# Kernel optimization log

Measured on AMD Instinct MI355X. Metric: run time of the kernel, lower is better.

Reference implementation:

```python
import jax, jax.numpy as jnp
import numpy as np

N, E, G = 50000, 800000, 64          # nodes, edges, graphs in batch
H, C = 4, 32                          # heads, per-head channels
D = H * C                             # 128 = gat_hidden_dim * n_heads
EMB = 16
IN_DIM = 2 * EMB + 1                  # 33
LSTM_H = 256
OUT = 4
V_LAB, V_TYP = 1000, 100
EPS = 1e-5


def _gatv2(x, src, dst, Wl, bl, Wr, br, att, bias):
    # GATv2Conv (PyG semantics, self-loops already appended to src/dst).
    xl = (x @ Wl + bl).reshape(-1, H, C)   # lin_l -> source-side messages x_j
    xr = (x @ Wr + br).reshape(-1, H, C)   # lin_r -> target-side x_i
    xj = xl[src]                            # [Et, H, C]
    e = jax.nn.leaky_relu(xr[dst] + xj, 0.2)
    score = jnp.einsum('ehc,hc->eh', e, att)             # [Et, H]
    smax = jax.ops.segment_max(score, dst, num_segments=N)
    a = jnp.exp(score - smax[dst])
    denom = jax.ops.segment_sum(a, dst, num_segments=N)
    alpha = a / denom[dst]                                # scatter-softmax per dst
    out = jax.ops.segment_sum(xj * alpha[:, :, None], dst, num_segments=N)
    return out.reshape(N, D) + bias


def _graph_norm(x, batch_ids, w, b, ms):
    # PyG GraphNorm: per-graph mean (scaled by learnable ms) and variance.
    cnt = jax.ops.segment_sum(jnp.ones((N,), x.dtype), batch_ids, num_segments=G)[:, None]
    mean = jax.ops.segment_sum(x, batch_ids, num_segments=G) / cnt
    out = x - mean[batch_ids] * ms
    var = jax.ops.segment_sum(out * out, batch_ids, num_segments=G) / cnt
    return w * out / jnp.sqrt(var + EPS)[batch_ids] + b


def _lstm0(x, Wih, Whh, bih, bhh):
    # Single LSTM time-step with h0 = c0 = 0: the Whh @ h0 term vanishes,
    # the forget gate multiplies c0 = 0.  Gate order (PyTorch): i, f, g, o.
    g = x @ Wih.T + bih + bhh
    i, f, gg, o = jnp.split(g, 4, axis=-1)
    c = jax.nn.sigmoid(i) * jnp.tanh(gg)
    return jax.nn.sigmoid(o) * jnp.tanh(c)


def setup_inputs() -> dict:
    key = jax.random.key(0)
    ks = jax.random.split(key, 32)
    rn = lambda k, s, sc=0.05: jax.random.normal(k, s, jnp.float32) * sc
    Z4 = LSTM_H * 4
    return {
        'node_labels': jax.random.randint(ks[0], (N,), 0, V_LAB, jnp.int32),
        'node_types': jax.random.randint(ks[1], (N,), 0, V_TYP, jnp.int32),
        'node_feat': jax.random.normal(ks[2], (N, 1), jnp.float32),
        'edge_index': jax.random.randint(ks[3], (2, E), 0, N, jnp.int32),
        'batch_ids': jnp.sort(jax.random.randint(ks[4], (N,), 0, G, jnp.int32)),
        'emb_label': rn(ks[5], (V_LAB, EMB), 1.0),
        'emb_type': rn(ks[6], (V_TYP, EMB), 1.0),
        'W_in': rn(ks[7], (IN_DIM, D)), 'b_in': jnp.zeros((D,), jnp.float32),
        'g1_Wl': rn(ks[8], (D, D)), 'g1_bl': jnp.zeros((D,), jnp.float32),
        'g1_Wr': rn(ks[9], (D, D)), 'g1_br': jnp.zeros((D,), jnp.float32),
        'g1_att': rn(ks[10], (H, C), 0.1), 'g1_bias': jnp.zeros((D,), jnp.float32),
        'gn1_w': jnp.ones((D,), jnp.float32), 'gn1_b': jnp.zeros((D,), jnp.float32),
        'gn1_ms': jnp.ones((D,), jnp.float32),
        'g2_Wl': rn(ks[11], (D, D)), 'g2_bl': jnp.zeros((D,), jnp.float32),
        'g2_Wr': rn(ks[12], (D, D)), 'g2_br': jnp.zeros((D,), jnp.float32),
        'g2_att': rn(ks[13], (H, C), 0.1), 'g2_bias': jnp.zeros((D,), jnp.float32),
        'gn2_w': jnp.ones((D,), jnp.float32), 'gn2_b': jnp.zeros((D,), jnp.float32),
        'gn2_ms': jnp.ones((D,), jnp.float32),
        'W_res': rn(ks[14], (D, D)), 'b_res': jnp.zeros((D,), jnp.float32),
        'l1_Wih': rn(ks[15], (Z4, D)), 'l1_Whh': rn(ks[16], (Z4, LSTM_H)),
        'l1_bih': jnp.zeros((Z4,), jnp.float32), 'l1_bhh': jnp.zeros((Z4,), jnp.float32),
        'l2_Wih': rn(ks[17], (Z4, LSTM_H)), 'l2_Whh': rn(ks[18], (Z4, LSTM_H)),
        'l2_bih': jnp.zeros((Z4,), jnp.float32), 'l2_bhh': jnp.zeros((Z4,), jnp.float32),
        'ln_w': jnp.ones((LSTM_H,), jnp.float32), 'ln_b': jnp.zeros((LSTM_H,), jnp.float32),
        'fc_W': rn(ks[19], (LSTM_H, OUT)), 'fc_b': jnp.zeros((OUT,), jnp.float32),
    }


def reference(node_labels, node_types, node_feat, edge_index, batch_ids,
              emb_label, emb_type, W_in, b_in,
              g1_Wl, g1_bl, g1_Wr, g1_br, g1_att, g1_bias, gn1_w, gn1_b, gn1_ms,
              g2_Wl, g2_bl, g2_Wr, g2_br, g2_att, g2_bias, gn2_w, gn2_b, gn2_ms,
              W_res, b_res,
              l1_Wih, l1_Whh, l1_bih, l1_bhh, l2_Wih, l2_Whh, l2_bih, l2_bhh,
              ln_w, ln_b, fc_W, fc_b):
    # Node features: [label_emb | type_emb | scalar]  -> [N, 33]
    feat = jnp.concatenate([emb_label[node_labels], emb_type[node_types], node_feat], axis=1)
    # PositionalEncoding at position 0 with odd d_model=33 adds exactly zeros (no-op).
    x = feat @ W_in + b_in                                  # [N, D]

    loops = jnp.arange(N, dtype=edge_index.dtype)           # GATv2Conv add_self_loops=True
    src = jnp.concatenate([edge_index[0], loops])
    dst = jnp.concatenate([edge_index[1], loops])

    x1 = jax.nn.elu(_graph_norm(_gatv2(x, src, dst, g1_Wl, g1_bl, g1_Wr, g1_br, g1_att, g1_bias),
                                batch_ids, gn1_w, gn1_b, gn1_ms))
    # dropout = identity in eval mode
    x2 = jax.nn.elu(_graph_norm(_gatv2(x1, src, dst, g2_Wl, g2_bl, g2_Wr, g2_br, g2_att, g2_bias),
                                batch_ids, gn2_w, gn2_b, gn2_ms) + x1 @ W_res + b_res)

    h1 = _lstm0(x2, l1_Wih, l1_Whh, l1_bih, l1_bhh)         # seq_len = 1 LSTM
    h2 = _lstm0(h1, l2_Wih, l2_Whh, l2_bih, l2_bhh)

    mu = h2.mean(-1, keepdims=True)
    var = ((h2 - mu) ** 2).mean(-1, keepdims=True)
    hn = ln_w * (h2 - mu) / jnp.sqrt(var + EPS) + ln_b      # LayerNorm

    cnt = jax.ops.segment_sum(jnp.ones((N,), hn.dtype), batch_ids, num_segments=G)[:, None]
    pooled = jax.ops.segment_sum(hn, batch_ids, num_segments=G) / cnt  # global_mean_pool
    return jax.nn.log_softmax(pooled @ fc_W + fc_b, axis=1)            # [G, OUT]
```

## Files before the change

### kernel.cpp

```cpp
#include <hip/hip_runtime.h>
#include <cstdint>
#include <cstddef>

#define DD 128
#define LSTMH 256
#define ZG 1024

typedef __attribute__((ext_vector_type(8))) short short8v;
typedef __attribute__((ext_vector_type(4))) float float4v;

static inline int cdiv_(int a, int b) { return (a + b - 1) / b; }

__device__ __forceinline__ float sigm_(float x) { return 1.f / (1.f + __expf(-x)); }
__device__ __forceinline__ float tanh_(float x) {
  float e = __expf(-2.f * fabsf(x));
  float r = (1.f - e) / (1.f + e);
  return copysignf(r, x);
}

__device__ __forceinline__ unsigned short f2bf(float f) {
  uint32_t u = __float_as_uint(f);
  u += 0x7fffu + ((u >> 16) & 1u);
  return (unsigned short)(u >> 16);
}
__device__ __forceinline__ uint32_t bfpack(float a, float b) {
  return (uint32_t)f2bf(a) | ((uint32_t)f2bf(b) << 16);
}
__device__ __forceinline__ float bflo(uint32_t u) { return __uint_as_float(u << 16); }
__device__ __forceinline__ float bfhi(uint32_t u) { return __uint_as_float(u & 0xffff0000u); }

__global__ void prep_all(const float* __restrict__ g1Wl, const float* __restrict__ g1Wr,
                         const float* __restrict__ g2Wl, const float* __restrict__ g2Wr,
                         const float* __restrict__ Wres, const float* __restrict__ l1Wih,
                         const float* __restrict__ l2Wih, const float* __restrict__ g1bl,
                         const float* __restrict__ g1br, const float* __restrict__ g2bl,
                         const float* __restrict__ g2br, const float* __restrict__ bres,
                         const float* __restrict__ l1bih, const float* __restrict__ l1bhh,
                         const float* __restrict__ l2bih, const float* __restrict__ l2bhh,
                         unsigned short* __restrict__ wcat1, unsigned short* __restrict__ wcat2,
                         unsigned short* __restrict__ wl1b, unsigned short* __restrict__ wl2b,
                         float* __restrict__ bcat1, float* __restrict__ bcat2,
                         float* __restrict__ bsum1, float* __restrict__ bsum2) {
  int i = blockIdx.x * 256 + threadIdx.x;
  if (i < 81920) {
    int seg = i >> 14, j = i & 16383;
    int m = j >> 7, k = j & 127;
    const float* src = (seg == 0) ? g1Wl : (seg == 1) ? g1Wr : (seg == 2) ? g2Wl
                       : (seg == 3) ? g2Wr : Wres;
    unsigned short* dst = (seg == 0) ? wcat1 : (seg == 1) ? wcat1 + 16384
                          : (seg == 2) ? wcat2 : (seg == 3) ? wcat2 + 16384 : wcat2 + 32768;
    dst[j] = f2bf(src[k * 128 + m]);
    return;
  }
  i -= 81920;
  if (i < 131072) { wl1b[i] = f2bf(l1Wih[i]); return; }
  i -= 131072;
  if (i < 262144) { wl2b[i] = f2bf(l2Wih[i]); return; }
  i -= 262144;
  if (i < 256) { bcat1[i] = (i < 128) ? g1bl[i] : g1br[i - 128]; return; }
  i -= 256;
  if (i < 384) {
    bcat2[i] = (i < 128) ? g2bl[i] : (i < 256 ? g2br[i - 128] : bres[i - 256]);
    return;
  }
  i -= 384;
  if (i < 1024) { bsum1[i] = l1bih[i] + l1bhh[i]; return; }
  i -= 1024;
  if (i < 1024) { bsum2[i] = l2bih[i] + l2bhh[i]; return; }
}

__global__ __launch_bounds__(256) void embed_in2(
    const int* __restrict__ labels, const int* __restrict__ types,
    const float* __restrict__ nf, const float* __restrict__ embL,
    const float* __restrict__ embT, const float* __restrict__ W,
    const float* __restrict__ b, unsigned short* __restrict__ x, int N) {
  __shared__ float f[128][34];
  int base = blockIdx.x * 128;
  int tid = threadIdx.x;
  int ch = tid & 127, half = tid >> 7;
  float wr[33];
#pragma unroll
  for (int k = 0; k < 33; ++k) wr[k] = W[k * 128 + ch];
  float bb = b[ch];
  int nmax = N - base < 128 ? N - base : 128;
  for (int e = tid; e < nmax * 32; e += 256) {
    int n = e >> 5, k = e & 31;
    f[n][k] = (k < 16) ? embL[labels[base + n] * 16 + k] : embT[types[base + n] * 16 + (k - 16)];
  }
  for (int n = tid; n < nmax; n += 256) f[n][32] = nf[base + n];
  __syncthreads();
  for (int n = half; n < nmax; n += 2) {
    float acc = bb;
#pragma unroll
    for (int k = 0; k < 33; ++k) acc = fmaf(f[n][k], wr[k], acc);
    x[(size_t)(base + n) * 128 + ch] = f2bf(acc);
  }
}

__global__ void count_deg(const int* __restrict__ ei, int* __restrict__ deg, int E_, int N_) {
  int i = blockIdx.x * 256 + threadIdx.x;
  if (i < E_) atomicAdd(&deg[ei[E_ + i]], 1);
  else if (i < E_ + N_) atomicAdd(&deg[i - E_], 1);
}

__global__ __launch_bounds__(256) void scan1(const int* __restrict__ deg, int* __restrict__ offs,
                                             int* __restrict__ partials, int N_) {
  __shared__ int buf[2][256];
  int tid = threadIdx.x;
  int i = blockIdx.x * 256 + tid;
  int v = (i < N_) ? deg[i] : 0;
  buf[0][tid] = v;
  __syncthreads();
  int cur = 0;
#pragma unroll
  for (int d = 1; d < 256; d <<= 1) {
    int xv = buf[cur][tid];
    if (tid >= d) xv += buf[cur][tid - d];
    buf[cur ^ 1][tid] = xv;
    cur ^= 1;
    __syncthreads();
  }
  int incl = buf[cur][tid];
  if (i < N_) offs[i] = incl - v;
  if (tid == 255) partials[blockIdx.x] = incl;
}

__global__ __launch_bounds__(256) void scan2(int* __restrict__ partials, int* __restrict__ offs,
                                             int nb, int N_) {
  __shared__ int buf[2][256];
  int tid = threadIdx.x;
  int v = (tid < nb) ? partials[tid] : 0;
  buf[0][tid] = v;
  __syncthreads();
  int cur = 0;
#pragma unroll
  for (int d = 1; d < 256; d <<= 1) {
    int xv = buf[cur][tid];
    if (tid >= d) xv += buf[cur][tid - d];
    buf[cur ^ 1][tid] = xv;
    cur ^= 1;
    __syncthreads();
  }
  int incl = buf[cur][tid];
  if (tid < nb) partials[tid] = incl - v;
  if (tid == 255) offs[N_] = incl;
}

__global__ void scan3(int* __restrict__ offs, const int* __restrict__ partials, int N_) {
  int i = blockIdx.x * 256 + threadIdx.x;
  if (i < N_) offs[i] += partials[blockIdx.x];
}

__global__ void fill_csr(const int* __restrict__ ei, const int* __restrict__ offs,
                         int* __restrict__ cursor, int* __restrict__ csr, int E_, int N_) {
  int i = blockIdx.x * 256 + threadIdx.x;
  int s, d;
  if (i < E_) { s = ei[i]; d = ei[E_ + i]; }
  else if (i < E_ + N_) { s = d = i - E_; }
  else return;
  int pos = offs[d] + atomicAdd(&cursor[d], 1);
  csr[pos] = s;
}

__global__ void graph_ranges(const int* __restrict__ bids, int* __restrict__ gstart,
                             float* __restrict__ invcnt, int N_, int G_) {
  int t = threadIdx.x;
  if (t <= G_) {
    int lo = 0, hi = N_;
    while (lo < hi) { int mid = (lo + hi) >> 1; if (bids[mid] < t) lo = mid + 1; else hi = mid; }
    gstart[t] = lo;
  }
  __syncthreads();
  if (t < G_) {
    int c = gstart[t + 1] - gstart[t];
    invcnt[t] = (c > 0) ? 1.f / (float)c : 0.f;
  }
}

__global__ __launch_bounds__(256) void gemm_bf16(
    const unsigned short* __restrict__ A, const unsigned short* __restrict__ Bp,
    const float* __restrict__ bias, unsigned short* __restrict__ C, int M, int K, int Ncols) {
  __shared__ unsigned short As[128 * 40];
  __shared__ unsigned short Bs[128 * 40];
  int tid = threadIdx.x;
  int lane = tid & 63;
  int wid = tid >> 6;
  int rowBase = blockIdx.y * 128, colBase = blockIdx.x * 128;
  int wr = (wid >> 1) * 64, wc = (wid & 1) * 64;
  int fr = lane & 15, fg = lane >> 4;
  float4v acc[4][4];
#pragma unroll
  for (int i = 0; i < 4; ++i)
#pragma unroll
    for (int j = 0; j < 4; ++j) acc[i][j] = (float4v){0.f, 0.f, 0.f, 0.f};

  int sr = tid >> 2;
  int sc = tid & 3;
  int off_lo = (sc < 2) ? 32 * sc : 32 * sc - 56;

  for (int k0 = 0; k0 < K; k0 += 32) {
#pragma unroll
    for (int it = 0; it < 2; ++it) {
      int r = it * 64 + sr;
      uint4 va = make_uint4(0u, 0u, 0u, 0u);
      if (rowBase + r < M)
        va = *(const uint4*)(A + (size_t)(rowBase + r) * K + k0 + sc * 8);
      char* arow = (char*)(As + r * 40);
      *(uint2*)(arow + off_lo) = make_uint2(va.x, va.y);
      *(uint2*)(arow + off_lo + 16) = make_uint2(va.z, va.w);
      uint4 vb = *(const uint4*)(Bp + (size_t)(colBase + r) * K + k0 + sc * 8);
      char* brow = (char*)(Bs + r * 40);
      *(uint2*)(brow + off_lo) = make_uint2(vb.x, vb.y);
      *(uint2*)(brow + off_lo + 16) = make_uint2(vb.z, vb.w);
    }
    __syncthreads();
    short8v af[4], bfv[4];
#pragma unroll
    for (int i = 0; i < 4; ++i)
      af[i] = *(const short8v*)((const char*)As + (wr + 16 * i + fr) * 80 + fg * 16);
#pragma unroll
    for (int j = 0; j < 4; ++j)
      bfv[j] = *(const short8v*)((const char*)Bs + (wc + 16 * j + fr) * 80 + fg * 16);
#pragma unroll
    for (int i = 0; i < 4; ++i)
#pragma unroll
      for (int j = 0; j < 4; ++j)
        acc[i][j] = __builtin_amdgcn_mfma_f32_16x16x32_bf16(af[i], bfv[j], acc[i][j], 0, 0, 0);
    __syncthreads();
  }
#pragma unroll
  for (int j = 0; j < 4; ++j) {
    int gc = colBase + wc + 16 * j + fr;
    float bv = bias[gc];
#pragma unroll
    for (int i = 0; i < 4; ++i) {
      int gr0 = rowBase + wr + 16 * i + fg * 4;
#pragma unroll
      for (int rg = 0; rg < 4; ++rg) {
        int gr = gr0 + rg;
        if (gr < M) C[(size_t)gr * Ncols + gc] = f2bf(acc[i][j][rg] + bv);
      }
    }
  }
}

__global__ __launch_bounds__(256) void gat_agg(
    const unsigned short* __restrict__ xlr, int stride,
    const int* __restrict__ csr, const int* __restrict__ offs,
    const float* __restrict__ att, const float* __restrict__ bias,
    unsigned short* __restrict__ out, int N) {
  int wid = (blockIdx.x * 256 + threadIdx.x) >> 6;
  if (wid >= N) return;
  int lane = threadIdx.x & 63;
  int q = lane >> 4, ql = lane & 15;
  float4 aA = *(const float4*)&att[ql * 8];
  float4 aB = *(const float4*)&att[ql * 8 + 4];
  uint4 ur = *(const uint4*)(xlr + (size_t)wid * stride + 128 + ql * 8);
  float r0 = bflo(ur.x), r1 = bfhi(ur.x), r2 = bflo(ur.y), r3 = bfhi(ur.y);
  float r4 = bflo(ur.z), r5 = bfhi(ur.z), r6 = bflo(ur.w), r7 = bfhi(ur.w);
  float m = -1e30f, L = 0.f;
  float s0 = 0.f, s1 = 0.f, s2 = 0.f, s3 = 0.f, s4 = 0.f, s5 = 0.f, s6 = 0.f, s7 = 0.f;
  int js = offs[wid], je = offs[wid + 1];
  for (int j = js + q; j < je; j += 4) {
    int s = csr[j];
    uint4 u = *(const uint4*)(xlr + (size_t)s * stride + ql * 8);
    float x0 = bflo(u.x), x1 = bfhi(u.x), x2 = bflo(u.y), x3 = bfhi(u.y);
    float x4 = bflo(u.z), x5 = bfhi(u.z), x6 = bflo(u.w), x7 = bfhi(u.w);
    float v0 = fmaxf(r0 + x0, 0.2f * (r0 + x0));
    float v1 = fmaxf(r1 + x1, 0.2f * (r1 + x1));
    float v2 = fmaxf(r2 + x2, 0.2f * (r2 + x2));
    float v3 = fmaxf(r3 + x3, 0.2f * (r3 + x3));
    float v4 = fmaxf(r4 + x4, 0.2f * (r4 + x4));
    float v5 = fmaxf(r5 + x5, 0.2f * (r5 + x5));
    float v6 = fmaxf(r6 + x6, 0.2f * (r6 + x6));
    float v7 = fmaxf(r7 + x7, 0.2f * (r7 + x7));
    float p = aA.x * v0 + aA.y * v1 + aA.z * v2 + aA.w * v3 +
              aB.x * v4 + aB.y * v5 + aB.z * v6 + aB.w * v7;
    p += __shfl_xor(p, 1); p += __shfl_xor(p, 2);
    float mn = fmaxf(m, p);
    float ea = __expf(p - mn);
    float es = __expf(m - mn);
    L = L * es + ea;
    s0 = s0 * es + ea * x0; s1 = s1 * es + ea * x1;
    s2 = s2 * es + ea * x2; s3 = s3 * es + ea * x3;
    s4 = s4 * es + ea * x4; s5 = s5 * es + ea * x5;
    s6 = s6 * es + ea * x6; s7 = s7 * es + ea * x7;
    m = mn;
  }
#pragma unroll
  for (int d = 16; d <= 32; d <<= 1) {
    float mo = __shfl_xor(m, d), Lo = __shfl_xor(L, d);
    float t0 = __shfl_xor(s0, d), t1 = __shfl_xor(s1, d);
    float t2 = __shfl_xor(s2, d), t3 = __shfl_xor(s3, d);
    float t4 = __shfl_xor(s4, d), t5 = __shfl_xor(s5, d);
    float t6 = __shfl_xor(s6, d), t7 = __shfl_xor(s7, d);
    float mn = fmaxf(m, mo);
    float e0 = __expf(m - mn), e1 = __expf(mo - mn);
    L = L * e0 + Lo * e1;
    s0 = s0 * e0 + t0 * e1; s1 = s1 * e0 + t1 * e1;
    s2 = s2 * e0 + t2 * e1; s3 = s3 * e0 + t3 * e1;
    s4 = s4 * e0 + t4 * e1; s5 = s5 * e0 + t5 * e1;
    s6 = s6 * e0 + t6 * e1; s7 = s7 * e0 + t7 * e1;
    m = mn;
  }
  if (q == 0) {
    float inv = 1.f / L;
    float4 bA = *(const float4*)&bias[ql * 8];
    float4 bB = *(const float4*)&bias[ql * 8 + 4];
    uint4 ov;
    ov.x = bfpack(s0 * inv + bA.x, s1 * inv + bA.y);
    ov.y = bfpack(s2 * inv + bA.z, s3 * inv + bA.w);
    ov.z = bfpack(s4 * inv + bB.x, s5 * inv + bB.y);
    ov.w = bfpack(s6 * inv + bB.z, s7 * inv + bB.w);
    *(uint4*)(out + (size_t)wid * DD + ql * 8) = ov;
  }
}

__global__ __launch_bounds__(256) void gn_stats2(const unsigned short* __restrict__ x,
                                                 const int* __restrict__ bids,
                                                 float* __restrict__ gsum,
                                                 float* __restrict__ gsq, int N) {
  int base = blockIdx.x * 128;
  int cp = threadIdx.x & 63;
  int sub = threadIdx.x >> 6;
  int end = base + 128 < N ? base + 128 : N;
  int curg = -1;
  float s0 = 0.f, s1 = 0.f, q0 = 0.f, q1 = 0.f;
  for (int r = base + sub; r < end; r += 4) {
    int g = bids[r];
    if (g != curg) {
      if (curg >= 0) {
        atomicAdd(&gsum[curg * DD + cp * 2], s0);
        atomicAdd(&gsum[curg * DD + cp * 2 + 1], s1);
        atomicAdd(&gsq[curg * DD + cp * 2], q0);
        atomicAdd(&gsq[curg * DD + cp * 2 + 1], q1);
      }
      curg = g; s0 = s1 = q0 = q1 = 0.f;
    }
    uint32_t u = *(const uint32_t*)(x + (size_t)r * DD + cp * 2);
    float v0 = bflo(u), v1 = bfhi(u);
    s0 += v0; q0 += v0 * v0; s1 += v1; q1 += v1 * v1;
  }
  if (curg >= 0) {
    atomicAdd(&gsum[curg * DD + cp * 2], s0);
    atomicAdd(&gsum[curg * DD + cp * 2 + 1], s1);
    atomicAdd(&gsq[curg * DD + cp * 2], q0);
    atomicAdd(&gsq[curg * DD + cp * 2 + 1], q1);
  }
}

template <bool ADDRES>
__global__ void gn_apply(const unsigned short* __restrict__ xin,
                         unsigned short* __restrict__ xout,
                         const unsigned short* __restrict__ res, int resStride,
                         const int* __restrict__ bids, const float* __restrict__ gsum,
                         const float* __restrict__ gsq, const float* __restrict__ invcnt,
                         const float* __restrict__ w, const float* __restrict__ b,
                         const float* __restrict__ ms, int N) {
  int idx = blockIdx.x * 256 + threadIdx.x;
  if (idx >= N * 64) return;
  int n = idx >> 6, cp = idx & 63;
  int g = bids[n];
  float ic = invcnt[g];
  float2 sm = *(const float2*)&gsum[g * DD + cp * 2];
  float2 sq = *(const float2*)&gsq[g * DD + cp * 2];
  float2 w2 = *(const float2*)&w[cp * 2];
  float2 b2 = *(const float2*)&b[cp * 2];
  float2 m2 = *(const float2*)&ms[cp * 2];
  uint32_t u = *(const uint32_t*)(xin + (size_t)n * DD + cp * 2);
  float mean0 = sm.x * ic, mean1 = sm.y * ic;
  float mm0 = mean0 * m2.x, mm1 = mean1 * m2.y;
  float var0 = sq.x * ic - mm0 * (2.f * mean0 - mm0);
  float var1 = sq.y * ic - mm1 * (2.f * mean1 - mm1);
  float v0 = (bflo(u) - mm0) * rsqrtf(var0 + 1e-5f) * w2.x + b2.x;
  float v1 = (bfhi(u) - mm1) * rsqrtf(var1 + 1e-5f) * w2.y + b2.y;
  if (ADDRES) {
    uint32_t ur = *(const uint32_t*)(res + (size_t)n * resStride + cp * 2);
    v0 += bflo(ur); v1 += bfhi(ur);
  }
  v0 = v0 > 0.f ? v0 : (__expf(v0) - 1.f);
  v1 = v1 > 0.f ? v1 : (__expf(v1) - 1.f);
  *(uint32_t*)(xout + (size_t)n * DD + cp * 2) = bfpack(v0, v1);
}

template <int KD>
__global__ __launch_bounds__(512, 4) void lstm_big(
    const unsigned short* __restrict__ A, const unsigned short* __restrict__ Bp,
    const float* __restrict__ bsum, unsigned short* __restrict__ H, int M) {
  __shared__ __attribute__((aligned(16))) char As_[128 * 272];
  __shared__ __attribute__((aligned(16))) char Ws_[96 * 272];
  const int NPH = KD / 128;
  int npanel = (M + 127) >> 7;
  int b = blockIdx.x;
  int g8 = b & 7, inner = b >> 3;
  int p = g8 + 8 * (inner >> 3);
  int cc = inner & 7;
  if (p >= npanel) return;
  int rowBase = p << 7;
  int ch0 = cc * 32;

  int tid = threadIdx.x;
  int lane = tid & 63;
  int wid = tid >> 6;
  int wr4 = wid >> 1;
  int wc2 = wid & 1;
  int fr = lane & 15, fg = lane >> 4;

  int ar[4], ac[4], asc[4], aolo[4], aldst[4];
#pragma unroll
  for (int q = 0; q < 4; ++q) {
    int e = q * 512 + tid;
    int r = e >> 4, kk = e & 15;
    int c = kk >> 2, sc = kk & 3;
    ar[q] = r; ac[q] = c; asc[q] = sc;
    aolo[q] = (sc < 2) ? 32 * sc : 32 * sc - 56;
    aldst[q] = r * 272 + c * 64;
  }
  int wgrow[3], wc_[3], wsc[3], wolo[3], wldst[3];
#pragma unroll
  for (int q = 0; q < 3; ++q) {
    int e = q * 512 + tid;
    int wrow = e >> 4, kk = e & 15;
    int c = kk >> 2, sc = kk & 3;
    int half = wrow >= 48 ? 1 : 0;
    int r3 = wrow - 48 * half;
    int grp = r3 >> 4;
    int goff = (grp == 0) ? 0 : (grp == 1 ? 512 : 768);
    wgrow[q] = goff + ch0 + 16 * half + (r3 & 15);
    wc_[q] = c; wsc[q] = sc;
    wolo[q] = (sc < 2) ? 32 * sc : 32 * sc - 56;
    wldst[q] = wrow * 272 + c * 64;
  }

  float4v acc[2][3];
#pragma unroll
  for (int i = 0; i < 2; ++i)
#pragma unroll
    for (int j = 0; j < 3; ++j) acc[i][j] = (float4v){0.f, 0.f, 0.f, 0.f};

  uint4 va[4], vw[3];
#pragma unroll
  for (int q = 0; q < 4; ++q) {
    va[q] = make_uint4(0u, 0u, 0u, 0u);
    if (rowBase + ar[q] < M)
      va[q] = *(const uint4*)(A + (size_t)(rowBase + ar[q]) * KD + ac[q] * 32 + asc[q] * 8);
  }
#pragma unroll
  for (int q = 0; q < 3; ++q)
    vw[q] = *(const uint4*)(Bp + (size_t)wgrow[q] * KD + wc_[q] * 32 + wsc[q] * 8);

#pragma unroll
  for (int ph = 0; ph < NPH; ++ph) {
    if (ph) __syncthreads();
#pragma unroll
    for (int q = 0; q < 4; ++q) {
      char* dst = As_ + aldst[q];
      *(uint2*)(dst + aolo[q]) = make_uint2(va[q].x, va[q].y);
      *(uint2*)(dst + aolo[q] + 16) = make_uint2(va[q].z, va[q].w);
    }
#pragma unroll
    for (int q = 0; q < 3; ++q) {
      char* dst = Ws_ + wldst[q];
      *(uint2*)(dst + wolo[q]) = make_uint2(vw[q].x, vw[q].y);
      *(uint2*)(dst + wolo[q] + 16) = make_uint2(vw[q].z, vw[q].w);
    }
    __syncthreads();
    if (ph + 1 < NPH) {
      int koff = (ph + 1) * 128;
#pragma unroll
      for (int q = 0; q < 4; ++q) {
        va[q] = make_uint4(0u, 0u, 0u, 0u);
        if (rowBase + ar[q] < M)
          va[q] = *(const uint4*)(A + (size_t)(rowBase + ar[q]) * KD + koff + ac[q] * 32 + asc[q] * 8);
      }
#pragma unroll
      for (int q = 0; q < 3; ++q)
        vw[q] = *(const uint4*)(Bp + (size_t)wgrow[q] * KD + koff + wc_[q] * 32 + wsc[q] * 8);
    }
    __builtin_amdgcn_s_setprio(1);
#pragma unroll
    for (int c = 0; c < 4; ++c) {
      short8v af[2], bf[3];
#pragma unroll
      for (int i = 0; i < 2; ++i)
        af[i] = *(const short8v*)(As_ + (32 * wr4 + 16 * i + fr) * 272 + c * 64 + fg * 16);
#pragma unroll
      for (int j = 0; j < 3; ++j)
        bf[j] = *(const short8v*)(Ws_ + (48 * wc2 + 16 * j + fr) * 272 + c * 64 + fg * 16);
#pragma unroll
      for (int i = 0; i < 2; ++i)
#pragma unroll
        for (int j = 0; j < 3; ++j)
          acc[i][j] = __builtin_amdgcn_mfma_f32_16x16x32_bf16(af[i], bf[j], acc[i][j], 0, 0, 0);
    }
    __builtin_amdgcn_s_setprio(0);
  }
  int chL = 16 * wc2 + fr;
  int ch = ch0 + chL;
  float bi = bsum[ch], bg = bsum[512 + ch], bo = bsum[768 + ch];
  unsigned short hv[8];
#pragma unroll
  for (int i = 0; i < 2; ++i) {
#pragma unroll
    for (int rg = 0; rg < 4; ++rg) {
      float iv = acc[i][0][rg] + bi;
      float gv = acc[i][1][rg] + bg;
      float ov = acc[i][2][rg] + bo;
      float c = sigm_(iv) * tanh_(gv);
      hv[i * 4 + rg] = f2bf(sigm_(ov) * tanh_(c));
    }
  }
  __syncthreads();
  unsigned short* Hs = (unsigned short*)As_;
#pragma unroll
  for (int i = 0; i < 2; ++i) {
#pragma unroll
    for (int rg = 0; rg < 4; ++rg) {
      int row = 32 * wr4 + 16 * i + 4 * fg + rg;
      Hs[row * 40 + chL] = hv[i * 4 + rg];
    }
  }
  __syncthreads();
  {
    int row = tid >> 2, seg = tid & 3;
    if (rowBase + row < M) {
      uint4 v = *(const uint4*)(Hs + row * 40 + seg * 8);
      *(uint4*)(H + (size_t)(rowBase + row) * LSTMH + ch0 + seg * 8) = v;
    }
  }
}

__global__ __launch_bounds__(256) void ln_pool2(
    const unsigned short* __restrict__ h2, const int* __restrict__ bids,
    const float* __restrict__ lnw, const float* __restrict__ lnb,
    const float* __restrict__ invcnt, float* __restrict__ pooled, int N) {
  int wave = (blockIdx.x * 256 + threadIdx.x) >> 6;
  int lane = threadIdx.x & 63;
  int r0 = wave * 8;
  if (r0 >= N) return;
  float4 w4 = *(const float4*)&lnw[lane * 4];
  float4 b4 = *(const float4*)&lnb[lane * 4];
  float p0 = 0.f, p1 = 0.f, p2 = 0.f, p3 = 0.f;
  int curg = bids[r0];
  int rend = r0 + 8 < N ? r0 + 8 : N;
  for (int r = r0; r < rend; ++r) {
    int g = bids[r];
    if (g != curg) {
      float ic = invcnt[curg];
      atomicAdd(&pooled[curg * LSTMH + lane * 4 + 0], p0 * ic);
      atomicAdd(&pooled[curg * LSTMH + lane * 4 + 1], p1 * ic);
      atomicAdd(&pooled[curg * LSTMH + lane * 4 + 2], p2 * ic);
      atomicAdd(&pooled[curg * LSTMH + lane * 4 + 3], p3 * ic);
      p0 = p1 = p2 = p3 = 0.f;
      curg = g;
    }
    uint2 u = *(const uint2*)(h2 + (size_t)r * LSTMH + lane * 4);
    float v0 = bflo(u.x), v1 = bfhi(u.x), v2 = bflo(u.y), v3 = bfhi(u.y);
    float s = v0 + v1 + v2 + v3;
    float q = v0 * v0 + v1 * v1 + v2 * v2 + v3 * v3;
#pragma unroll
    for (int d = 1; d < 64; d <<= 1) { s += __shfl_xor(s, d); q += __shfl_xor(q, d); }
    float mu = s * (1.f / 256.f);
    float var = q * (1.f / 256.f) - mu * mu;
    float rs = rsqrtf(var + 1e-5f);
    p0 += w4.x * (v0 - mu) * rs + b4.x;
    p1 += w4.y * (v1 - mu) * rs + b4.y;
    p2 += w4.z * (v2 - mu) * rs + b4.z;
    p3 += w4.w * (v3 - mu) * rs + b4.w;
  }
  float ic = invcnt[curg];
  atomicAdd(&pooled[curg * LSTMH + lane * 4 + 0], p0 * ic);
  atomicAdd(&pooled[curg * LSTMH + lane * 4 + 1], p1 * ic);
  atomicAdd(&pooled[curg * LSTMH + lane * 4 + 2], p2 * ic);
  atomicAdd(&pooled[curg * LSTMH + lane * 4 + 3], p3 * ic);
}

__global__ __launch_bounds__(64) void fc_lsm(const float* __restrict__ pooled,
                                             const float* __restrict__ W,
                                             const float* __restrict__ b, float* __restrict__ out) {
  int g = blockIdx.x;
  int t = threadIdx.x;
  float l0 = 0.f, l1 = 0.f, l2 = 0.f, l3 = 0.f;
  for (int k = t; k < LSTMH; k += 64) {
    float p = pooled[g * LSTMH + k];
    l0 += p * W[k * 4 + 0];
    l1 += p * W[k * 4 + 1];
    l2 += p * W[k * 4 + 2];
    l3 += p * W[k * 4 + 3];
  }
#pragma unroll
  for (int d = 1; d < 64; d <<= 1) {
    l0 += __shfl_xor(l0, d); l1 += __shfl_xor(l1, d);
    l2 += __shfl_xor(l2, d); l3 += __shfl_xor(l3, d);
  }
  if (t == 0) {
    float z[4] = {l0 + b[0], l1 + b[1], l2 + b[2], l3 + b[3]};
    float mx = fmaxf(fmaxf(z[0], z[1]), fmaxf(z[2], z[3]));
    float sum = __expf(z[0] - mx) + __expf(z[1] - mx) + __expf(z[2] - mx) + __expf(z[3] - mx);
    float ls = logf(sum);
#pragma unroll
    for (int o = 0; o < 4; ++o) out[g * 4 + o] = z[o] - mx - ls;
  }
}

extern "C" void kernel_launch(void* const* d_in, const int* in_sizes, int n_in,
                              void* d_out, int out_size, void* d_ws, size_t ws_size,
                              hipStream_t stream) {
  const int* node_labels = (const int*)d_in[0];
  const int* node_types = (const int*)d_in[1];
  const float* node_feat = (const float*)d_in[2];
  const int* edge_index = (const int*)d_in[3];
  const int* batch_ids = (const int*)d_in[4];
  const float* emb_label = (const float*)d_in[5];
  const float* emb_type = (const float*)d_in[6];
  const float* W_in = (const float*)d_in[7];
  const float* b_in = (const float*)d_in[8];
  const float* g1_Wl = (const float*)d_in[9];
  const float* g1_bl = (const float*)d_in[10];
  const float* g1_Wr = (const float*)d_in[11];
  const float* g1_br = (const float*)d_in[12];
  const float* g1_att = (const float*)d_in[13];
  const float* g1_bias = (const float*)d_in[14];
  const float* gn1_w = (const float*)d_in[15];
  const float* gn1_b = (const float*)d_in[16];
  const float* gn1_ms = (const float*)d_in[17];
  const float* g2_Wl = (const float*)d_in[18];
  const float* g2_bl = (const float*)d_in[19];
  const float* g2_Wr = (const float*)d_in[20];
  const float* g2_br = (const float*)d_in[21];
  const float* g2_att = (const float*)d_in[22];
  const float* g2_bias = (const float*)d_in[23];
  const float* gn2_w = (const float*)d_in[24];
  const float* gn2_b = (const float*)d_in[25];
  const float* gn2_ms = (const float*)d_in[26];
  const float* W_res = (const float*)d_in[27];
  const float* b_res = (const float*)d_in[28];
  const float* l1_Wih = (const float*)d_in[29];
  const float* l1_bih = (const float*)d_in[31];
  const float* l1_bhh = (const float*)d_in[32];
  const float* l2_Wih = (const float*)d_in[33];
  const float* l2_bih = (const float*)d_in[35];
  const float* l2_bhh = (const float*)d_in[36];
  const float* ln_w = (const float*)d_in[37];
  const float* ln_b = (const float*)d_in[38];
  const float* fc_W = (const float*)d_in[39];
  const float* fc_b = (const float*)d_in[40];
  float* out = (float*)d_out;

  const int N = in_sizes[0];
  const int E = in_sizes[3] / 2;
  const int G = out_size / 4;
  const int ET = E + N;

  char* wsb = (char*)d_ws;
  size_t off = 0;
  auto alloc = [&](size_t bytes) -> void* {
    void* p = (void*)(wsb + off);
    off = (off + bytes + 255) & ~(size_t)255;
    return p;
  };
  unsigned short* xA = (unsigned short*)alloc((size_t)N * 512);
  unsigned short* xb = (unsigned short*)alloc((size_t)N * DD * 2);
  unsigned short* xlr = (unsigned short*)alloc((size_t)N * 384 * 2);
  int* deg = (int*)alloc((size_t)N * 4);
  int* offs = (int*)alloc((size_t)(N + 1) * 4);
  int* cursor = (int*)alloc((size_t)N * 4);
  int* partials = (int*)alloc(1024);
  int* csr = (int*)alloc((size_t)ET * 4);
  int* gstart = (int*)alloc((size_t)(G + 1) * 4);
  float* invcnt = (float*)alloc((size_t)G * 4);
  float* gsum = (float*)alloc((size_t)G * DD * 4);
  float* gsq = (float*)alloc((size_t)G * DD * 4);
  float* pooled = (float*)alloc((size_t)G * LSTMH * 4);
  float* bcat1 = (float*)alloc(256 * 4);
  float* bcat2 = (float*)alloc(384 * 4);
  float* bsum1 = (float*)alloc(ZG * 4);
  float* bsum2 = (float*)alloc(ZG * 4);
  unsigned short* wcat1 = (unsigned short*)alloc((size_t)256 * DD * 2);
  unsigned short* wcat2 = (unsigned short*)alloc((size_t)384 * DD * 2);
  unsigned short* wl1b = (unsigned short*)alloc((size_t)ZG * DD * 2);
  unsigned short* wl2b = (unsigned short*)alloc((size_t)ZG * LSTMH * 2);
  (void)ws_size; (void)n_in;

  unsigned short* h1 = xlr;
  unsigned short* h2 = xA;

  hipMemsetAsync(deg, 0, (size_t)N * 4, stream);
  hipMemsetAsync(cursor, 0, (size_t)N * 4, stream);
  hipMemsetAsync(pooled, 0, (size_t)G * LSTMH * 4, stream);

  prep_all<<<1867, 256, 0, stream>>>(g1_Wl, g1_Wr, g2_Wl, g2_Wr, W_res, l1_Wih, l2_Wih,
                                     g1_bl, g1_br, g2_bl, g2_br, b_res, l1_bih, l1_bhh,
                                     l2_bih, l2_bhh, wcat1, wcat2, wl1b, wl2b,
                                     bcat1, bcat2, bsum1, bsum2);
  graph_ranges<<<1, 128, 0, stream>>>(batch_ids, gstart, invcnt, N, G);
  embed_in2<<<cdiv_(N, 128), 256, 0, stream>>>(node_labels, node_types, node_feat, emb_label,
                                               emb_type, W_in, b_in, xb, N);

  count_deg<<<cdiv_(ET, 256), 256, 0, stream>>>(edge_index, deg, E, N);
  int nb1 = cdiv_(N, 256);
  scan1<<<nb1, 256, 0, stream>>>(deg, offs, partials, N);
  scan2<<<1, 256, 0, stream>>>(partials, offs, nb1, N);
  scan3<<<nb1, 256, 0, stream>>>(offs, partials, N);
  fill_csr<<<cdiv_(ET, 256), 256, 0, stream>>>(edge_index, offs, cursor, csr, E, N);

  int mb = cdiv_(N, 128);
  gemm_bf16<<<dim3(2, mb), 256, 0, stream>>>(xb, wcat1, bcat1, xlr, N, DD, 256);
  gat_agg<<<cdiv_(N, 4), 256, 0, stream>>>(xlr, 256, csr, offs, g1_att, g1_bias, xA, N);
  hipMemsetAsync(gsum, 0, (size_t)G * DD * 8, stream);
  gn_stats2<<<cdiv_(N, 128), 256, 0, stream>>>(xA, batch_ids, gsum, gsq, N);
  gn_apply<false><<<cdiv_(N * 64, 256), 256, 0, stream>>>(
      xA, xb, nullptr, 0, batch_ids, gsum, gsq, invcnt, gn1_w, gn1_b, gn1_ms, N);
  gemm_bf16<<<dim3(3, mb), 256, 0, stream>>>(xb, wcat2, bcat2, xlr, N, DD, 384);
  gat_agg<<<cdiv_(N, 4), 256, 0, stream>>>(xlr, 384, csr, offs, g2_att, g2_bias, xA, N);
  hipMemsetAsync(gsum, 0, (size_t)G * DD * 8, stream);
  gn_stats2<<<cdiv_(N, 128), 256, 0, stream>>>(xA, batch_ids, gsum, gsq, N);
  gn_apply<true><<<cdiv_(N * 64, 256), 256, 0, stream>>>(
      xA, xb, xlr + 256, 384, batch_ids, gsum, gsq, invcnt, gn2_w, gn2_b, gn2_ms, N);
  int npanel = cdiv_(N, 128);
  int lblocks = 64 * cdiv_(npanel, 8);
  lstm_big<DD><<<lblocks, 512, 0, stream>>>(xb, wl1b, bsum1, h1, N);
  lstm_big<LSTMH><<<lblocks, 512, 0, stream>>>(h1, wl2b, bsum2, h2, N);
  ln_pool2<<<cdiv_(N, 32), 256, 0, stream>>>(h2, batch_ids, ln_w, ln_b, invcnt, pooled, N);
  fc_lsm<<<G, 64, 0, stream>>>(pooled, fc_W, fc_b, out);
}
```

Measured before the change: 487.0 us.

## Fold memsets into kernels and shrink LSTM GEMM K-phase tiles

Removes the separate hipMemsetAsync calls. prep_all now zeroes deg, cursor and pooled, and gat_agg zeroes the GraphNorm accumulators (gsum/gsq) from its first 4096 threads. The LSTM GEMM kernel now stages K in 64-wide phases instead of 128, which halves its shared-memory tiles, and its launch bound rises to 6 blocks per CU. This trades more barrier phases for higher occupancy and fewer launches.

```diff
diff --git a/kernel.cpp b/kernel.cpp
--- a/kernel.cpp
+++ b/kernel.cpp
@@ -40,7 +40,9 @@
                          unsigned short* __restrict__ wcat1, unsigned short* __restrict__ wcat2,
                          unsigned short* __restrict__ wl1b, unsigned short* __restrict__ wl2b,
                          float* __restrict__ bcat1, float* __restrict__ bcat2,
-                         float* __restrict__ bsum1, float* __restrict__ bsum2) {
+                         float* __restrict__ bsum1, float* __restrict__ bsum2,
+                         int* __restrict__ deg, int* __restrict__ cursor,
+                         float* __restrict__ pooled, int Nn) {
   int i = blockIdx.x * 256 + threadIdx.x;
   if (i < 81920) {
     int seg = i >> 14, j = i & 16383;
@@ -67,6 +69,12 @@
   if (i < 1024) { bsum1[i] = l1bih[i] + l1bhh[i]; return; }
   i -= 1024;
   if (i < 1024) { bsum2[i] = l2bih[i] + l2bhh[i]; return; }
+  i -= 1024;
+  if (i < Nn) { deg[i] = 0; return; }
+  i -= Nn;
+  if (i < Nn) { cursor[i] = 0; return; }
+  i -= Nn;
+  if (i < 16384) { pooled[i] = 0.f; return; }
 }
 
 __global__ __launch_bounds__(256) void embed_in2(
@@ -248,8 +256,10 @@
     const unsigned short* __restrict__ xlr, int stride,
     const int* __restrict__ csr, const int* __restrict__ offs,
     const float* __restrict__ att, const float* __restrict__ bias,
-    unsigned short* __restrict__ out, int N) {
-  int wid = (blockIdx.x * 256 + threadIdx.x) >> 6;
+    unsigned short* __restrict__ out, float* __restrict__ gz, int N) {
+  int zt = blockIdx.x * 256 + threadIdx.x;
+  if (zt < 4096) *(float4*)(gz + zt * 4) = make_float4(0.f, 0.f, 0.f, 0.f);
+  int wid = zt >> 6;
   if (wid >= N) return;
   int lane = threadIdx.x & 63;
   int q = lane >> 4, ql = lane & 15;
@@ -384,12 +394,12 @@
 }
 
 template <int KD>
-__global__ __launch_bounds__(512, 4) void lstm_big(
+__global__ __launch_bounds__(512, 6) void lstm_big(
     const unsigned short* __restrict__ A, const unsigned short* __restrict__ Bp,
     const float* __restrict__ bsum, unsigned short* __restrict__ H, int M) {
-  __shared__ __attribute__((aligned(16))) char As_[128 * 272];
-  __shared__ __attribute__((aligned(16))) char Ws_[96 * 272];
-  const int NPH = KD / 128;
+  __shared__ __attribute__((aligned(16))) char As_[128 * 136];
+  __shared__ __attribute__((aligned(16))) char Ws_[96 * 136];
+  const int NPH = KD / 64;
   int npanel = (M + 127) >> 7;
   int b = blockIdx.x;
   int g8 = b & 7, inner = b >> 3;
@@ -406,30 +416,33 @@
   int wc2 = wid & 1;
   int fr = lane & 15, fg = lane >> 4;
 
-  int ar[4], ac[4], asc[4], aolo[4], aldst[4];
-#pragma unroll
-  for (int q = 0; q < 4; ++q) {
+  int aldst[2], agoff[2];
+  bool aval[2];
+#pragma unroll
+  for (int q = 0; q < 2; ++q) {
     int e = q * 512 + tid;
-    int r = e >> 4, kk = e & 15;
+    int r = e >> 3, kk = e & 7;
     int c = kk >> 2, sc = kk & 3;
-    ar[q] = r; ac[q] = c; asc[q] = sc;
-    aolo[q] = (sc < 2) ? 32 * sc : 32 * sc - 56;
-    aldst[q] = r * 272 + c * 64;
-  }
-  int wgrow[3], wc_[3], wsc[3], wolo[3], wldst[3];
-#pragma unroll
-  for (int q = 0; q < 3; ++q) {
+    int olo = (sc < 2) ? 32 * sc : 32 * sc - 56;
+    aldst[q] = r * 136 + c * 64 + olo;
+    aval[q] = (rowBase + r) < M;
+    agoff[q] = (rowBase + r) * KD + c * 32 + sc * 8;
+  }
+  bool wact1 = tid < 256;
+  int wldst[2], wgoff[2];
+#pragma unroll
+  for (int q = 0; q < 2; ++q) {
     int e = q * 512 + tid;
-    int wrow = e >> 4, kk = e & 15;
+    int wrow = e >> 3, kk = e & 7;
     int c = kk >> 2, sc = kk & 3;
     int half = wrow >= 48 ? 1 : 0;
     int r3 = wrow - 48 * half;
     int grp = r3 >> 4;
     int goff = (grp == 0) ? 0 : (grp == 1 ? 512 : 768);
-    wgrow[q] = goff + ch0 + 16 * half + (r3 & 15);
-    wc_[q] = c; wsc[q] = sc;
-    wolo[q] = (sc < 2) ? 32 * sc : 32 * sc - 56;
-    wldst[q] = wrow * 272 + c * 64;
+    int grow = goff + ch0 + 16 * half + (r3 & 15);
+    int olo = (sc < 2) ? 32 * sc : 32 * sc - 56;
+    wldst[q] = wrow * 136 + c * 64 + olo;
+    wgoff[q] = grow * KD + c * 32 + sc * 8;
   }
 
   float4v acc[2][3];
@@ -438,55 +451,55 @@
 #pragma unroll
     for (int j = 0; j < 3; ++j) acc[i][j] = (float4v){0.f, 0.f, 0.f, 0.f};
 
-  uint4 va[4], vw[3];
-#pragma unroll
-  for (int q = 0; q < 4; ++q) {
+  uint4 va[2], vw[2];
+#pragma unroll
+  for (int q = 0; q < 2; ++q) {
     va[q] = make_uint4(0u, 0u, 0u, 0u);
-    if (rowBase + ar[q] < M)
-      va[q] = *(const uint4*)(A + (size_t)(rowBase + ar[q]) * KD + ac[q] * 32 + asc[q] * 8);
-  }
-#pragma unroll
-  for (int q = 0; q < 3; ++q)
-    vw[q] = *(const uint4*)(Bp + (size_t)wgrow[q] * KD + wc_[q] * 32 + wsc[q] * 8);
+    if (aval[q]) va[q] = *(const uint4*)(A + agoff[q]);
+  }
+  vw[0] = *(const uint4*)(Bp + wgoff[0]);
+  if (wact1) vw[1] = *(const uint4*)(Bp + wgoff[1]);
 
 #pragma unroll
   for (int ph = 0; ph < NPH; ++ph) {
     if (ph) __syncthreads();
 #pragma unroll
-    for (int q = 0; q < 4; ++q) {
+    for (int q = 0; q < 2; ++q) {
       char* dst = As_ + aldst[q];
-      *(uint2*)(dst + aolo[q]) = make_uint2(va[q].x, va[q].y);
-      *(uint2*)(dst + aolo[q] + 16) = make_uint2(va[q].z, va[q].w);
-    }
-#pragma unroll
-    for (int q = 0; q < 3; ++q) {
-      char* dst = Ws_ + wldst[q];
-      *(uint2*)(dst + wolo[q]) = make_uint2(vw[q].x, vw[q].y);
-      *(uint2*)(dst + wolo[q] + 16) = make_uint2(vw[q].z, vw[q].w);
+      *(uint2*)(dst) = make_uint2(va[q].x, va[q].y);
+      *(uint2*)(dst + 16) = make_uint2(va[q].z, va[q].w);
+    }
+    {
+      char* dst = Ws_ + wldst[0];
+      *(uint2*)(dst) = make_uint2(vw[0].x, vw[0].y);
+      *(uint2*)(dst + 16) = make_uint2(vw[0].z, vw[0].w);
+    }
+    if (wact1) {
+      char* dst = Ws_ + wldst[1];
+      *(uint2*)(dst) = make_uint2(vw[1].x, vw[1].y);
+      *(uint2*)(dst + 16) = make_uint2(vw[1].z, vw[1].w);
     }
     __syncthreads();
     if (ph + 1 < NPH) {
-      int koff = (ph + 1) * 128;
-#pragma unroll
-      for (int q = 0; q < 4; ++q) {
+      int koff = (ph + 1) * 64;
+#pragma unroll
+      for (int q = 0; q < 2; ++q) {
         va[q] = make_uint4(0u, 0u, 0u, 0u);
-        if (rowBase + ar[q] < M)
-          va[q] = *(const uint4*)(A + (size_t)(rowBase + ar[q]) * KD + koff + ac[q] * 32 + asc[q] * 8);
+        if (aval[q]) va[q] = *(const uint4*)(A + agoff[q] + koff);
       }
-#pragma unroll
-      for (int q = 0; q < 3; ++q)
-        vw[q] = *(const uint4*)(Bp + (size_t)wgrow[q] * KD + koff + wc_[q] * 32 + wsc[q] * 8);
+      vw[0] = *(const uint4*)(Bp + wgoff[0] + koff);
+      if (wact1) vw[1] = *(const uint4*)(Bp + wgoff[1] + koff);
     }
     __builtin_amdgcn_s_setprio(1);
 #pragma unroll
-    for (int c = 0; c < 4; ++c) {
+    for (int c = 0; c < 2; ++c) {
       short8v af[2], bf[3];
 #pragma unroll
       for (int i = 0; i < 2; ++i)
-        af[i] = *(const short8v*)(As_ + (32 * wr4 + 16 * i + fr) * 272 + c * 64 + fg * 16);
+        af[i] = *(const short8v*)(As_ + (32 * wr4 + 16 * i + fr) * 136 + c * 64 + fg * 16);
 #pragma unroll
       for (int j = 0; j < 3; ++j)
-        bf[j] = *(const short8v*)(Ws_ + (48 * wc2 + 16 * j + fr) * 272 + c * 64 + fg * 16);
+        bf[j] = *(const short8v*)(Ws_ + (48 * wc2 + 16 * j + fr) * 136 + c * 64 + fg * 16);
 #pragma unroll
       for (int i = 0; i < 2; ++i)
 #pragma unroll
@@ -685,14 +698,12 @@
   unsigned short* h1 = xlr;
   unsigned short* h2 = xA;
 
-  hipMemsetAsync(deg, 0, (size_t)N * 4, stream);
-  hipMemsetAsync(cursor, 0, (size_t)N * 4, stream);
-  hipMemsetAsync(pooled, 0, (size_t)G * LSTMH * 4, stream);
-
-  prep_all<<<1867, 256, 0, stream>>>(g1_Wl, g1_Wr, g2_Wl, g2_Wr, W_res, l1_Wih, l2_Wih,
-                                     g1_bl, g1_br, g2_bl, g2_br, b_res, l1_bih, l1_bhh,
-                                     l2_bih, l2_bhh, wcat1, wcat2, wl1b, wl2b,
-                                     bcat1, bcat2, bsum1, bsum2);
+  int prepTotal = 477824 + 2 * N + 16384;
+  prep_all<<<cdiv_(prepTotal, 256), 256, 0, stream>>>(
+      g1_Wl, g1_Wr, g2_Wl, g2_Wr, W_res, l1_Wih, l2_Wih,
+      g1_bl, g1_br, g2_bl, g2_br, b_res, l1_bih, l1_bhh, l2_bih, l2_bhh,
+      wcat1, wcat2, wl1b, wl2b, bcat1, bcat2, bsum1, bsum2,
+      deg, cursor, pooled, N);
   graph_ranges<<<1, 128, 0, stream>>>(batch_ids, gstart, invcnt, N, G);
   embed_in2<<<cdiv_(N, 128), 256, 0, stream>>>(node_labels, node_types, node_feat, emb_label,
                                                emb_type, W_in, b_in, xb, N);
@@ -706,14 +717,12 @@
 
   int mb = cdiv_(N, 128);
   gemm_bf16<<<dim3(2, mb), 256, 0, stream>>>(xb, wcat1, bcat1, xlr, N, DD, 256);
-  gat_agg<<<cdiv_(N, 4), 256, 0, stream>>>(xlr, 256, csr, offs, g1_att, g1_bias, xA, N);
-  hipMemsetAsync(gsum, 0, (size_t)G * DD * 8, stream);
+  gat_agg<<<cdiv_(N, 4), 256, 0, stream>>>(xlr, 256, csr, offs, g1_att, g1_bias, xA, gsum, N);
   gn_stats2<<<cdiv_(N, 128), 256, 0, stream>>>(xA, batch_ids, gsum, gsq, N);
   gn_apply<false><<<cdiv_(N * 64, 256), 256, 0, stream>>>(
       xA, xb, nullptr, 0, batch_ids, gsum, gsq, invcnt, gn1_w, gn1_b, gn1_ms, N);
   gemm_bf16<<<dim3(3, mb), 256, 0, stream>>>(xb, wcat2, bcat2, xlr, N, DD, 384);
-  gat_agg<<<cdiv_(N, 4), 256, 0, stream>>>(xlr, 384, csr, offs, g2_att, g2_bias, xA, N);
-  hipMemsetAsync(gsum, 0, (size_t)G * DD * 8, stream);
+  gat_agg<<<cdiv_(N, 4), 256, 0, stream>>>(xlr, 384, csr, offs, g2_att, g2_bias, xA, gsum, N);
   gn_stats2<<<cdiv_(N, 128), 256, 0, stream>>>(xA, batch_ids, gsum, gsq, N);
   gn_apply<true><<<cdiv_(N * 64, 256), 256, 0, stream>>>(
       xA, xb, xlr + 256, 384, batch_ids, gsum, gsq, invcnt, gn2_w, gn2_b, gn2_ms, N);
```

Result: faster. 476.7 us (-2.1%).
